# Kernel optimization log

Measured on AMD Instinct MI355X. Metric: run time of the kernel, lower is better.

Reference implementation:

```python
import jax, jax.numpy as jnp
import numpy as np

D = 25
H = W = D + 1           # 26x26 grid
L = D * D - 1           # 624 syndrome nodes
DD = 128                # d_d
CH = 256                # conv channels per layer
NL = 4                  # L_layers
B = 256
LN_EPS = 1e-5


def setup_inputs() -> dict:
    key = jax.random.key(0)
    ks = jax.random.split(key, 8)
    X = jax.random.normal(ks[0], (B, L, DD), dtype=jnp.float32)
    # distinct random grid cells for the coord <-> index bijection
    perm = jax.random.permutation(ks[1], H * W)[:L]
    coords = jnp.stack([perm // W, perm % W], axis=-1).astype(jnp.int32)  # [L,2]
    P = jnp.zeros((DD,), dtype=jnp.float32)
    ln_scale = jnp.ones((NL, DD), dtype=jnp.float32)
    ln_bias = jnp.zeros((NL, DD), dtype=jnp.float32)
    w3 = jax.random.normal(ks[2], (NL, 3, 3, DD, CH), dtype=jnp.float32) * 0.02  # HWIO
    b3 = jnp.zeros((NL, CH), dtype=jnp.float32)
    w1 = jax.random.normal(ks[3], (NL, CH, DD), dtype=jnp.float32) * 0.02  # 1x1 conv as matmul
    b1 = jnp.zeros((NL, DD), dtype=jnp.float32)
    return {"X": X, "coords": coords, "P": P, "ln_scale": ln_scale,
            "ln_bias": ln_bias, "w3": w3, "b3": b3, "w1": w1, "b1": b1}


def _layernorm(x, scale, bias):
    m = jnp.mean(x, axis=-1, keepdims=True)
    xc = x - m
    v = jnp.mean(xc * xc, axis=-1, keepdims=True)
    return xc * jax.lax.rsqrt(v + LN_EPS) * scale + bias


def reference(X, coords, P, ln_scale, ln_bias, w3, b3, w1, b1):
    Bb = X.shape[0]
    rows, cols = coords[:, 0], coords[:, 1]
    # scatter tokens onto the grid; empty cells hold learned padding P
    grid = jnp.broadcast_to(P, (Bb, H, W, DD))
    Y = grid.at[:, rows, cols, :].set(X)  # [B,H,W,DD], NHWC
    dn = jax.lax.conv_dimension_numbers(Y.shape, w3[0].shape, ('NHWC', 'HWIO', 'NHWC'))
    for l in range(NL):
        Yn = _layernorm(Y, ln_scale[l], ln_bias[l])
        Yn = jax.lax.conv_general_dilated(Yn, w3[l], window_strides=(1, 1),
                                          padding='SAME', rhs_dilation=(1, 1),
                                          dimension_numbers=dn) + b3[l]
        Yn = jax.nn.gelu(Yn, approximate=False)
        Yn = jnp.einsum('bhwc,cd->bhwd', Yn, w1[l]) + b1[l]  # 1x1 projection
        Y = Y + Yn
    # gather back to token sequence
    Z = Y[:, rows, cols, :]  # [B,L,DD]
    return Z
```

## Files before the change

kernel.cpp:

```cpp
#include <hip/hip_runtime.h>
#include <hip/hip_bf16.h>
#include <math.h>

#define Bsz 256
#define Hh 26
#define Ww 26
#define Ll 624
#define DDc 128
#define CHc 256
#define NLl 4
#define NPIX (Hh * Ww)
#define NROWS (Bsz * NPIX)
#define GRID_ELEMS (NROWS * DDc)

typedef short short8v __attribute__((ext_vector_type(8)));
typedef float f32x4 __attribute__((ext_vector_type(4)));
typedef unsigned short ushort4v __attribute__((ext_vector_type(4)));

__device__ __forceinline__ unsigned short f2bf(float f) {
    union { float f; unsigned int u; } v; v.f = f;
    unsigned int u = v.u;
    return (unsigned short)((u + 0x7FFFu + ((u >> 16) & 1u)) >> 16);
}

__device__ __forceinline__ float fast_gelu(float x) {
    float z = x * 0.70710678118654752f;
    float a = fabsf(z);
    float t = 1.0f / fmaf(0.3275911f, a, 1.0f);
    float p = fmaf(1.061405429f, t, -1.453152027f);
    p = fmaf(p, t, 1.421413741f);
    p = fmaf(p, t, -0.284496736f);
    p = fmaf(p, t, 0.254829592f);
    float e = __expf(-a * a);
    float y = fmaf(-p * t, e, 1.0f);
    float er = copysignf(y, z);
    return 0.5f * x * (1.0f + er);
}

__global__ void build_inv_kernel(const int* __restrict__ coords, int* __restrict__ inv) {
    int i = threadIdx.x;
    if (i < NPIX) inv[i] = -1;
    __syncthreads();
    if (i < Ll) {
        int r = coords[2 * i + 0];
        int c = coords[2 * i + 1];
        inv[r * Ww + c] = i;
    }
}

__global__ __launch_bounds__(256) void scatter_kernel(const float* __restrict__ X,
                                                      const float* __restrict__ P,
                                                      const int* __restrict__ inv,
                                                      float* __restrict__ Y) {
    int idx = blockIdx.x * blockDim.x + threadIdx.x;
    int r = idx >> 5;
    int c4 = idx & 31;
    int b = r / NPIX;
    int pos = r - b * NPIX;
    int li = inv[pos];
    float4 v;
    if (li >= 0) v = *(const float4*)(X + ((size_t)(b * Ll + li) * DDc + c4 * 4));
    else         v = *(const float4*)(P + c4 * 4);
    *(float4*)(Y + ((size_t)r * DDc + c4 * 4)) = v;
}

__global__ __launch_bounds__(256) void pack3_kernel(const float* __restrict__ w3,
                                                    unsigned short* __restrict__ w3f) {
    int g = blockIdx.x * 4 + (threadIdx.x >> 6);
    int lane = threadIdx.x & 63;
    int ks = g & 3;
    int nt = (g >> 2) & 15;
    int lt = g >> 6;
    int al = lane & 15, ah = lane >> 4;
    int n = nt * 16 + al;
    int k0 = ks * 32 + ah * 8;
    const float* src = w3 + ((size_t)lt * 128 + k0) * 256 + n;
    unsigned short* dst = w3f + ((size_t)g * 64 + lane) * 8;
#pragma unroll
    for (int e = 0; e < 8; ++e)
        dst[e] = f2bf(src[(size_t)e * 256]);
}

__global__ __launch_bounds__(256) void pack1_kernel(const float* __restrict__ w1,
                                                    unsigned short* __restrict__ w1f) {
    int g = blockIdx.x * 4 + (threadIdx.x >> 6);
    int lane = threadIdx.x & 63;
    int ks = g & 7;
    int nt = (g >> 3) & 7;
    int l = g >> 6;
    int al = lane & 15, ah = lane >> 4;
    int d = nt * 16 + al;
    int c0 = ks * 32 + ah * 8;
    const float* src = w1 + ((size_t)l * 256 + c0) * 128 + d;
    unsigned short* dst = w1f + ((size_t)g * 64 + lane) * 8;
#pragma unroll
    for (int e = 0; e < 8; ++e)
        dst[e] = f2bf(src[(size_t)e * 128]);
}

__global__ __launch_bounds__(256) void ln_kernel(const float* __restrict__ Y,
                                                 const float* __restrict__ scale,
                                                 const float* __restrict__ bias,
                                                 unsigned short* __restrict__ Yn) {
    int wave = threadIdx.x >> 6;
    int lane = threadIdx.x & 63;
    int r = blockIdx.x * 4 + wave;
    const float* yr = Y + (size_t)r * DDc;
    float2 v = *(const float2*)(yr + lane * 2);
    float s = v.x + v.y;
#pragma unroll
    for (int off = 32; off >= 1; off >>= 1) s += __shfl_xor(s, off, 64);
    float mean = s * (1.0f / 128.0f);
    float dx = v.x - mean, dy = v.y - mean;
    float s2 = dx * dx + dy * dy;
#pragma unroll
    for (int off = 32; off >= 1; off >>= 1) s2 += __shfl_xor(s2, off, 64);
    float rstd = rsqrtf(s2 * (1.0f / 128.0f) + 1e-5f);
    float2 sc = *(const float2*)(scale + lane * 2);
    float2 bi = *(const float2*)(bias + lane * 2);
    ushort2 o;
    o.x = f2bf(dx * rstd * sc.x + bi.x);
    o.y = f2bf(dy * rstd * sc.y + bi.y);
    *(ushort2*)(Yn + (size_t)r * DDc + lane * 2) = o;
}

#define Z_OFF 32768
#define LDS_TOTAL 33024

__global__ __launch_bounds__(256, 3) void conv_mfma_kernel(
    const unsigned short* __restrict__ Yn,
    const unsigned short* __restrict__ w3f,
    const float* __restrict__ b3l,
    const unsigned short* __restrict__ w1f,
    const float* __restrict__ b1l,
    float* __restrict__ Y) {
    __shared__ __align__(16) char lds[LDS_TOTAL];

    int bx = blockIdx.x;
    int b = bx / 13;
    int h0 = (bx - b * 13) * 2;
    int tid = threadIdx.x;
    int lane = tid & 63, wv = tid >> 6;
    int al = lane & 15, ah = lane >> 4;

    for (int i = tid; i < 4 * 28 * 16; i += 256) {
        int row4 = i / (28 * 16);
        int rem = i - row4 * (28 * 16);
        int col = rem >> 4;
        int c8 = (rem & 15) << 3;
        int hs = h0 - 1 + row4;
        int ws = col - 1;
        uint4 v = make_uint4(0u, 0u, 0u, 0u);
        if (hs >= 0 && hs < Hh && ws >= 0 && ws < Ww)
            v = *(const uint4*)(Yn + (((size_t)(b * Hh + hs) * Ww + ws) << 7) + c8);
        int r = row4 * 28 + col;
        unsigned int addr = (unsigned int)(r * 256 + c8 * 2);
        addr ^= (unsigned int)((r & 7) << 4);
        *(uint4*)(lds + addr) = v;
    }
    if (tid < 16) *(uint4*)(lds + Z_OFF + tid * 16) = make_uint4(0u, 0u, 0u, 0u);
    __syncthreads();

    int r00[4]; bool mpad[4];
#pragma unroll
    for (int mt = 0; mt < 4; ++mt) {
        int m = mt * 16 + al;
        bool pad = (m >= 52);
        int rh = (m >= 26) ? 1 : 0;
        int w = m - rh * 26;
        if (pad) { rh = 1; w = 0; }
        mpad[mt] = pad;
        r00[mt] = rh * 28 + w;
    }

    f32x4 acc[4][4];
#pragma unroll
    for (int mt = 0; mt < 4; ++mt)
#pragma unroll
        for (int nt = 0; nt < 4; ++nt) acc[mt][nt] = (f32x4)0.0f;

    int nw0 = wv * 64;
    const unsigned short* pB = w3f + wv * 8192 + lane * 8;
    const unsigned short* pBt = pB;

    unsigned int ah16 = (unsigned int)(ah * 16);
    unsigned int abase[4];
#pragma unroll
    for (int mt = 0; mt < 4; ++mt) {
        int row = r00[mt];
        unsigned int sw = (unsigned int)((row & 7) << 4);
        abase[mt] = mpad[mt] ? (unsigned int)(Z_OFF) + ah16
                             : ((unsigned int)(row << 8) + (ah16 ^ sw));
    }

    short8v bc[4], afc[4];
#pragma unroll
    for (int nt = 0; nt < 4; ++nt) bc[nt] = *(const short8v*)(pBt + nt * 2048);
#pragma unroll
    for (int mt = 0; mt < 4; ++mt) afc[mt] = *(const short8v*)(lds + abase[mt]);

    int dh = 0, dw = 0;
#pragma unroll 1
    for (int tap = 0; tap < 9; ++tap) {
        int dwn = dw + 1, dhn = dh;
        if (dwn == 3) { dwn = 0; dhn += 1; }
        unsigned int abasen[4];
#pragma unroll
        for (int mt = 0; mt < 4; ++mt) {
            int row = r00[mt] + dhn * 28 + dwn;
            if (row > 111) row = 111;
            unsigned int sw = (unsigned int)((row & 7) << 4);
            abasen[mt] = mpad[mt] ? (unsigned int)(Z_OFF) + ah16
                                  : ((unsigned int)(row << 8) + (ah16 ^ sw));
        }
#pragma unroll
        for (int ks = 0; ks < 4; ++ks) {
            short8v bn[4], afn[4];
            const unsigned short* pn = (ks < 3) ? (pBt + (ks + 1) * 512) : (pBt + 32768);
#pragma unroll
            for (int nt = 0; nt < 4; ++nt) bn[nt] = *(const short8v*)(pn + nt * 2048);
#pragma unroll
            for (int mt = 0; mt < 4; ++mt) {
                unsigned int a = (ks < 3) ? (abase[mt] ^ (unsigned int)((ks + 1) << 6))
                                          : abasen[mt];
                afn[mt] = *(const short8v*)(lds + a);
            }
            __builtin_amdgcn_sched_barrier(0);
#pragma unroll
            for (int mt = 0; mt < 4; ++mt)
#pragma unroll
                for (int nt = 0; nt < 4; ++nt)
                    acc[mt][nt] = __builtin_amdgcn_mfma_f32_16x16x32_bf16(
                        bc[nt], afc[mt], acc[mt][nt], 0, 0, 0);
#pragma unroll
            for (int nt = 0; nt < 4; ++nt) bc[nt] = bn[nt];
#pragma unroll
            for (int mt = 0; mt < 4; ++mt) afc[mt] = afn[mt];
        }
#pragma unroll
        for (int mt = 0; mt < 4; ++mt) abase[mt] = abasen[mt];
        pBt += 32768;
        dw = dwn; dh = dhn;
    }
    __syncthreads();

    unsigned int hswz = ((unsigned int)(al & 7)) << 4;
#pragma unroll
    for (int nt = 0; nt < 4; ++nt) {
        int n0 = nw0 + nt * 16 + ah * 4;
        float4 bv = *(const float4*)(b3l + n0);
#pragma unroll
        for (int mt = 0; mt < 4; ++mt) {
            int m = mt * 16 + al;
            ushort4v o;
            o[0] = f2bf(fast_gelu(acc[mt][nt][0] + bv.x));
            o[1] = f2bf(fast_gelu(acc[mt][nt][1] + bv.y));
            o[2] = f2bf(fast_gelu(acc[mt][nt][2] + bv.z));
            o[3] = f2bf(fast_gelu(acc[mt][nt][3] + bv.w));
            unsigned int addr = ((unsigned int)(m * 512 + n0 * 2)) ^ hswz;
            *(ushort4v*)(lds + addr) = o;
        }
    }
    __syncthreads();

    f32x4 acc1[4][2];
#pragma unroll
    for (int mt = 0; mt < 4; ++mt) { acc1[mt][0] = (f32x4)0.0f; acc1[mt][1] = (f32x4)0.0f; }
    const unsigned short* pW1 = w1f + wv * 8192 + lane * 8;
    int nw1 = wv * 32;

#pragma unroll
    for (int ks = 0; ks < 8; ++ks) {
        short8v hf[4], wf[2];
#pragma unroll
        for (int mt = 0; mt < 4; ++mt) {
            unsigned int a = ((unsigned int)((mt * 16 + al) * 512 + ks * 64 + ah * 16)) ^ hswz;
            hf[mt] = *(const short8v*)(lds + a);
        }
        wf[0] = *(const short8v*)(pW1 + ks * 512);
        wf[1] = *(const short8v*)(pW1 + 4096 + ks * 512);
#pragma unroll
        for (int mt = 0; mt < 4; ++mt)
#pragma unroll
            for (int ntl = 0; ntl < 2; ++ntl)
                acc1[mt][ntl] = __builtin_amdgcn_mfma_f32_16x16x32_bf16(
                    hf[mt], wf[ntl], acc1[mt][ntl], 0, 0, 0);
    }

#pragma unroll
    for (int ntl = 0; ntl < 2; ++ntl) {
        int n = nw1 + ntl * 16 + al;
        float bias = b1l[n];
#pragma unroll
        for (int mt = 0; mt < 4; ++mt) {
#pragma unroll
            for (int j = 0; j < 4; ++j) {
                int m = mt * 16 + ah * 4 + j;
                if (m < 52) {
                    int rh = (m >= 26) ? 1 : 0;
                    int w = m - rh * 26;
                    float* yp = Y + (((size_t)(b * Hh + h0 + rh) * Ww + w) << 7) + n;
                    *yp += acc1[mt][ntl][j] + bias;
                }
            }
        }
    }
}

__global__ __launch_bounds__(256) void gather_kernel(const float* __restrict__ Y,
                                                     const int* __restrict__ coords,
                                                     float* __restrict__ Z) {
    int idx = blockIdx.x * blockDim.x + threadIdx.x;
    int r = idx >> 5;
    int c4 = idx & 31;
    int b = r / Ll;
    int li = r - b * Ll;
    int row = coords[2 * li + 0];
    int col = coords[2 * li + 1];
    float4 v = *(const float4*)(Y + (((size_t)(b * NPIX + row * Ww + col)) * DDc + c4 * 4));
    *(float4*)(Z + ((size_t)r * DDc + c4 * 4)) = v;
}

extern "C" void kernel_launch(void* const* d_in, const int* in_sizes, int n_in,
                              void* d_out, int out_size, void* d_ws, size_t ws_size,
                              hipStream_t stream) {
    const float* X = (const float*)d_in[0];
    const int* coords = (const int*)d_in[1];
    const float* P = (const float*)d_in[2];
    const float* ln_scale = (const float*)d_in[3];
    const float* ln_bias = (const float*)d_in[4];
    const float* w3 = (const float*)d_in[5];
    const float* b3 = (const float*)d_in[6];
    const float* w1 = (const float*)d_in[7];
    const float* b1 = (const float*)d_in[8];

    float* Y = (float*)d_ws;
    unsigned short* Yn = (unsigned short*)(Y + GRID_ELEMS);
    unsigned short* w3f = Yn + GRID_ELEMS;
    unsigned short* w1f = w3f + (size_t)NLl * 9 * CHc * DDc;
    int* inv = (int*)(w1f + (size_t)NLl * DDc * CHc);

    build_inv_kernel<<<1, 1024, 0, stream>>>(coords, inv);

    pack3_kernel<<<(NLl * 9 * 16 * 4) / 4, 256, 0, stream>>>(w3, w3f);
    pack1_kernel<<<(NLl * 8 * 8) / 4, 256, 0, stream>>>(w1, w1f);

    scatter_kernel<<<(NROWS * 32) / 256, 256, 0, stream>>>(X, P, inv, Y);

    for (int l = 0; l < NLl; ++l) {
        ln_kernel<<<NROWS / 4, 256, 0, stream>>>(Y, ln_scale + l * DDc, ln_bias + l * DDc, Yn);
        conv_mfma_kernel<<<Bsz * 13, 256, 0, stream>>>(
            Yn,
            w3f + (size_t)l * 9 * CHc * DDc,
            b3 + (size_t)l * CHc,
            w1f + (size_t)l * DDc * CHc,
            b1 + (size_t)l * DDc,
            Y);
    }

    gather_kernel<<<(Bsz * Ll * 32) / 256, 256, 0, stream>>>(Y, coords, (float*)d_out);
}
```

Baseline: 906.6 us.

## Tile conv by 64 contiguous pixels with 8 waves per block

The fused conv kernel now gives each block 64 contiguous pixels of an image (11 blocks per image) instead of two grid rows padded from 52 to 64. This cuts the padded MFMA rows that did no useful work. Blocks grow to 512 threads (8 waves), each handling half as many output channels, and stage a 6-row halo tile in LDS. The trade is a larger LDS footprint and halo overhead per block, with fewer output channels per wave, which lowers register pressure but reduces reuse of A fragments.

```diff
diff --git a/kernel.cpp b/kernel.cpp
--- a/kernel.cpp
+++ b/kernel.cpp
@@ -12,6 +12,7 @@
 #define NPIX (Hh * Ww)
 #define NROWS (Bsz * NPIX)
 #define GRID_ELEMS (NROWS * DDc)
+#define PBLK 11
 
 typedef short short8v __attribute__((ext_vector_type(8)));
 typedef float f32x4 __attribute__((ext_vector_type(4)));
@@ -124,10 +125,10 @@
     *(ushort2*)(Yn + (size_t)r * DDc + lane * 2) = o;
 }
 
-#define Z_OFF 32768
-#define LDS_TOTAL 33024
-
-__global__ __launch_bounds__(256, 3) void conv_mfma_kernel(
+#define Z_OFF 43008
+#define LDS_TOTAL 43264
+
+__global__ __launch_bounds__(512, 4) void conv_mfma_kernel(
     const unsigned short* __restrict__ Yn,
     const unsigned short* __restrict__ w3f,
     const float* __restrict__ b3l,
@@ -137,23 +138,24 @@
     __shared__ __align__(16) char lds[LDS_TOTAL];
 
     int bx = blockIdx.x;
-    int b = bx / 13;
-    int h0 = (bx - b * 13) * 2;
+    int b = bx / PBLK;
+    int p0 = (bx - b * PBLK) * 64;
+    int r0 = (p0 * 2521) >> 16;
     int tid = threadIdx.x;
     int lane = tid & 63, wv = tid >> 6;
     int al = lane & 15, ah = lane >> 4;
 
-    for (int i = tid; i < 4 * 28 * 16; i += 256) {
-        int row4 = i / (28 * 16);
-        int rem = i - row4 * (28 * 16);
+    for (int i = tid; i < 6 * 28 * 16; i += 512) {
+        int row6 = i / (28 * 16);
+        int rem = i - row6 * (28 * 16);
         int col = rem >> 4;
         int c8 = (rem & 15) << 3;
-        int hs = h0 - 1 + row4;
+        int hs = r0 - 1 + row6;
         int ws = col - 1;
         uint4 v = make_uint4(0u, 0u, 0u, 0u);
         if (hs >= 0 && hs < Hh && ws >= 0 && ws < Ww)
             v = *(const uint4*)(Yn + (((size_t)(b * Hh + hs) * Ww + ws) << 7) + c8);
-        int r = row4 * 28 + col;
+        int r = row6 * 28 + col;
         unsigned int addr = (unsigned int)(r * 256 + c8 * 2);
         addr ^= (unsigned int)((r & 7) << 4);
         *(uint4*)(lds + addr) = v;
@@ -164,23 +166,21 @@
     int r00[4]; bool mpad[4];
 #pragma unroll
     for (int mt = 0; mt < 4; ++mt) {
-        int m = mt * 16 + al;
-        bool pad = (m >= 52);
-        int rh = (m >= 26) ? 1 : 0;
-        int w = m - rh * 26;
-        if (pad) { rh = 1; w = 0; }
+        int p = p0 + mt * 16 + al;
+        bool pad = (p >= NPIX);
+        int rh = (p * 2521) >> 16;
+        int w = p - rh * 26;
+        int srow = rh - r0;
+        if (pad) { srow = 0; w = 0; }
         mpad[mt] = pad;
-        r00[mt] = rh * 28 + w;
-    }
-
-    f32x4 acc[4][4];
-#pragma unroll
-    for (int mt = 0; mt < 4; ++mt)
-#pragma unroll
-        for (int nt = 0; nt < 4; ++nt) acc[mt][nt] = (f32x4)0.0f;
-
-    int nw0 = wv * 64;
-    const unsigned short* pB = w3f + wv * 8192 + lane * 8;
+        r00[mt] = srow * 28 + w;
+    }
+
+    f32x4 acc[4][2];
+#pragma unroll
+    for (int mt = 0; mt < 4; ++mt) { acc[mt][0] = (f32x4)0.0f; acc[mt][1] = (f32x4)0.0f; }
+
+    const unsigned short* pB = w3f + wv * 4096 + lane * 8;
     const unsigned short* pBt = pB;
 
     unsigned int ah16 = (unsigned int)(ah * 16);
@@ -193,9 +193,9 @@
                              : ((unsigned int)(row << 8) + (ah16 ^ sw));
     }
 
-    short8v bc[4], afc[4];
-#pragma unroll
-    for (int nt = 0; nt < 4; ++nt) bc[nt] = *(const short8v*)(pBt + nt * 2048);
+    short8v bc[2], afc[4];
+#pragma unroll
+    for (int g = 0; g < 2; ++g) bc[g] = *(const short8v*)(pBt + g * 2048);
 #pragma unroll
     for (int mt = 0; mt < 4; ++mt) afc[mt] = *(const short8v*)(lds + abase[mt]);
 
@@ -208,17 +208,17 @@
 #pragma unroll
         for (int mt = 0; mt < 4; ++mt) {
             int row = r00[mt] + dhn * 28 + dwn;
-            if (row > 111) row = 111;
+            if (row > 167) row = 167;
             unsigned int sw = (unsigned int)((row & 7) << 4);
             abasen[mt] = mpad[mt] ? (unsigned int)(Z_OFF) + ah16
                                   : ((unsigned int)(row << 8) + (ah16 ^ sw));
         }
 #pragma unroll
         for (int ks = 0; ks < 4; ++ks) {
-            short8v bn[4], afn[4];
+            short8v bn[2], afn[4];
             const unsigned short* pn = (ks < 3) ? (pBt + (ks + 1) * 512) : (pBt + 32768);
 #pragma unroll
-            for (int nt = 0; nt < 4; ++nt) bn[nt] = *(const short8v*)(pn + nt * 2048);
+            for (int g = 0; g < 2; ++g) bn[g] = *(const short8v*)(pn + g * 2048);
 #pragma unroll
             for (int mt = 0; mt < 4; ++mt) {
                 unsigned int a = (ks < 3) ? (abase[mt] ^ (unsigned int)((ks + 1) << 6))
@@ -229,11 +229,11 @@
 #pragma unroll
             for (int mt = 0; mt < 4; ++mt)
 #pragma unroll
-                for (int nt = 0; nt < 4; ++nt)
-                    acc[mt][nt] = __builtin_amdgcn_mfma_f32_16x16x32_bf16(
-                        bc[nt], afc[mt], acc[mt][nt], 0, 0, 0);
-#pragma unroll
-            for (int nt = 0; nt < 4; ++nt) bc[nt] = bn[nt];
+                for (int g = 0; g < 2; ++g)
+                    acc[mt][g] = __builtin_amdgcn_mfma_f32_16x16x32_bf16(
+                        bc[g], afc[mt], acc[mt][g], 0, 0, 0);
+#pragma unroll
+            for (int g = 0; g < 2; ++g) bc[g] = bn[g];
 #pragma unroll
             for (int mt = 0; mt < 4; ++mt) afc[mt] = afn[mt];
         }
@@ -246,61 +246,53 @@
 
     unsigned int hswz = ((unsigned int)(al & 7)) << 4;
 #pragma unroll
-    for (int nt = 0; nt < 4; ++nt) {
-        int n0 = nw0 + nt * 16 + ah * 4;
+    for (int g = 0; g < 2; ++g) {
+        int n0 = wv * 32 + g * 16 + ah * 4;
         float4 bv = *(const float4*)(b3l + n0);
 #pragma unroll
         for (int mt = 0; mt < 4; ++mt) {
             int m = mt * 16 + al;
             ushort4v o;
-            o[0] = f2bf(fast_gelu(acc[mt][nt][0] + bv.x));
-            o[1] = f2bf(fast_gelu(acc[mt][nt][1] + bv.y));
-            o[2] = f2bf(fast_gelu(acc[mt][nt][2] + bv.z));
-            o[3] = f2bf(fast_gelu(acc[mt][nt][3] + bv.w));
+            o[0] = f2bf(fast_gelu(acc[mt][g][0] + bv.x));
+            o[1] = f2bf(fast_gelu(acc[mt][g][1] + bv.y));
+            o[2] = f2bf(fast_gelu(acc[mt][g][2] + bv.z));
+            o[3] = f2bf(fast_gelu(acc[mt][g][3] + bv.w));
             unsigned int addr = ((unsigned int)(m * 512 + n0 * 2)) ^ hswz;
             *(ushort4v*)(lds + addr) = o;
         }
     }
     __syncthreads();
 
-    f32x4 acc1[4][2];
-#pragma unroll
-    for (int mt = 0; mt < 4; ++mt) { acc1[mt][0] = (f32x4)0.0f; acc1[mt][1] = (f32x4)0.0f; }
-    const unsigned short* pW1 = w1f + wv * 8192 + lane * 8;
-    int nw1 = wv * 32;
+    f32x4 acc1[4];
+#pragma unroll
+    for (int mt = 0; mt < 4; ++mt) acc1[mt] = (f32x4)0.0f;
+    const unsigned short* pW1 = w1f + wv * 4096 + lane * 8;
 
 #pragma unroll
     for (int ks = 0; ks < 8; ++ks) {
-        short8v hf[4], wf[2];
+        short8v hf[4], wf;
 #pragma unroll
         for (int mt = 0; mt < 4; ++mt) {
             unsigned int a = ((unsigned int)((mt * 16 + al) * 512 + ks * 64 + ah * 16)) ^ hswz;
             hf[mt] = *(const short8v*)(lds + a);
         }
-        wf[0] = *(const short8v*)(pW1 + ks * 512);
-        wf[1] = *(const short8v*)(pW1 + 4096 + ks * 512);
+        wf = *(const short8v*)(pW1 + ks * 512);
 #pragma unroll
         for (int mt = 0; mt < 4; ++mt)
-#pragma unroll
-            for (int ntl = 0; ntl < 2; ++ntl)
-                acc1[mt][ntl] = __builtin_amdgcn_mfma_f32_16x16x32_bf16(
-                    hf[mt], wf[ntl], acc1[mt][ntl], 0, 0, 0);
-    }
-
-#pragma unroll
-    for (int ntl = 0; ntl < 2; ++ntl) {
-        int n = nw1 + ntl * 16 + al;
-        float bias = b1l[n];
+            acc1[mt] = __builtin_amdgcn_mfma_f32_16x16x32_bf16(hf[mt], wf, acc1[mt], 0, 0, 0);
+    }
+
+    {
+        int d = wv * 16 + al;
+        float bias = b1l[d];
 #pragma unroll
         for (int mt = 0; mt < 4; ++mt) {
 #pragma unroll
             for (int j = 0; j < 4; ++j) {
-                int m = mt * 16 + ah * 4 + j;
-                if (m < 52) {
-                    int rh = (m >= 26) ? 1 : 0;
-                    int w = m - rh * 26;
-                    float* yp = Y + (((size_t)(b * Hh + h0 + rh) * Ww + w) << 7) + n;
-                    *yp += acc1[mt][ntl][j] + bias;
+                int p = p0 + mt * 16 + ah * 4 + j;
+                if (p < NPIX) {
+                    float* yp = Y + (((size_t)(b * NPIX + p)) << 7) + d;
+                    *yp += acc1[mt][j] + bias;
                 }
             }
         }
@@ -349,7 +341,7 @@
 
     for (int l = 0; l < NLl; ++l) {
         ln_kernel<<<NROWS / 4, 256, 0, stream>>>(Y, ln_scale + l * DDc, ln_bias + l * DDc, Yn);
-        conv_mfma_kernel<<<Bsz * 13, 256, 0, stream>>>(
+        conv_mfma_kernel<<<Bsz * PBLK, 512, 0, stream>>>(
             Yn,
             w3f + (size_t)l * 9 * CHc * DDc,
             b3 + (size_t)l * CHc,
```

Measured after the change: 933.4 us. 1.03x slower.
